# Kernel optimization log

Measured on AMD Instinct MI355X. Metric: run time of the kernel, lower is better.

## Reference

```python
import jax, jax.numpy as jnp
import numpy as np

Y_SCALE = 0.01  # fixed weight quantization scale (q_scale of the int8 weights)


def setup_inputs() -> dict:
    key = jax.random.key(0)
    kx, kw, kb = jax.random.split(key, 3)
    B, S, IN, OUT = 4, 2048, 4096, 4096
    x = jax.random.normal(kx, (B, S, IN), dtype=jnp.float32)
    # int8 quantized weights, stored transposed as (in_features, out_features)
    weight_q = jax.random.randint(kw, (IN, OUT), -128, 128, dtype=jnp.int32)
    bias = jax.random.normal(kb, (OUT,), dtype=jnp.float32)
    return {"x": x, "weight_q": weight_q, "bias": bias}


def reference(x, weight_q, bias):
    # Per-batch-sample dynamic activation scale: max(|x_i|)/128 over each [S, IN] slice
    x_scale = jnp.max(jnp.abs(x), axis=(1, 2), keepdims=True) / 128.0  # [B,1,1]
    # int8 quantize: round + clip
    xq = jnp.clip(jnp.round(x / x_scale), -128, 127).astype(jnp.int8)  # [B,S,IN]
    wq = weight_q.astype(jnp.int8)                                      # [IN,OUT]
    c = jax.lax.dot_general(
        xq, wq,
        dimension_numbers=(((2,), (0,)), ((), ())),
        preferred_element_type=jnp.int32,
    )  # [B,S,OUT]
    # dequantize and bias-add
    y = c.astype(jnp.float32) * (x_scale * Y_SCALE)
    return y + bias
```

## Files before the change

kernel.cpp:

```cpp
#include <hip/hip_runtime.h>
#include <stdint.h>

#define K_DIM 4096
#define N_DIM 4096
#define M_DIM 8192
#define S_ROWS 2048
#define NKT 64

typedef int v4i __attribute__((ext_vector_type(4)));

__device__ __forceinline__ void gload16(const void* g, void* l) {
    __builtin_amdgcn_global_load_lds(
        (const __attribute__((address_space(1))) unsigned int*)g,
        (__attribute__((address_space(3))) unsigned int*)l, 16, 0, 0);
}

__device__ __forceinline__ void barrier() {
    asm volatile("" ::: "memory");
    __builtin_amdgcn_s_barrier();
    asm volatile("" ::: "memory");
}

__global__ void prep1_kernel(const float* __restrict__ x, unsigned* __restrict__ amax,
                             const int* __restrict__ wq, char* __restrict__ wt) {
    __shared__ unsigned lds[64 * 17];
    if (blockIdx.x < 4096) {
        int b = blockIdx.x >> 10;
        int bx = blockIdx.x & 1023;
        const float4* xb = (const float4*)(x + (size_t)b * S_ROWS * K_DIM);
        int tid = bx * 256 + threadIdx.x;
        const int stride = 1024 * 256;
        float m = 0.f;
#pragma unroll
        for (int i = 0; i < 8; ++i) {
            float4 v = xb[tid + i * stride];
            m = fmaxf(m, fmaxf(fmaxf(fabsf(v.x), fabsf(v.y)),
                               fmaxf(fabsf(v.z), fabsf(v.w))));
        }
#pragma unroll
        for (int off = 32; off; off >>= 1)
            m = fmaxf(m, __shfl_xor(m, off));
        float* red = (float*)lds;
        if ((threadIdx.x & 63) == 0) red[threadIdx.x >> 6] = m;
        __syncthreads();
        if (threadIdx.x == 0) {
            m = fmaxf(fmaxf(red[0], red[1]), fmaxf(red[2], red[3]));
            atomicMax(&amax[b], __float_as_uint(m));
        }
    } else {
        int wb = blockIdx.x - 4096;
        int n0 = (wb & 63) * 64;
        int k0 = (wb >> 6) * 64;
        int t = threadIdx.x;
        int c = t & 63;
        int g = t >> 6;
#pragma unroll
        for (int rep = 0; rep < 4; ++rep) {
            int kb = g * 16 + rep * 4;
            int v0 = wq[(size_t)(k0 + kb + 0) * N_DIM + n0 + c];
            int v1 = wq[(size_t)(k0 + kb + 1) * N_DIM + n0 + c];
            int v2 = wq[(size_t)(k0 + kb + 2) * N_DIM + n0 + c];
            int v3 = wq[(size_t)(k0 + kb + 3) * N_DIM + n0 + c];
            lds[c * 17 + (kb >> 2)] =
                (v0 & 255) | ((v1 & 255) << 8) | ((v2 & 255) << 16) | ((v3 & 255) << 24);
        }
        __syncthreads();
        int row = t >> 2;
        int ch = t & 3;
        uint4 o;
        o.x = lds[row * 17 + ch * 4 + 0];
        o.y = lds[row * 17 + ch * 4 + 1];
        o.z = lds[row * 17 + ch * 4 + 2];
        o.w = lds[row * 17 + ch * 4 + 3];
        *(uint4*)(wt + (size_t)(n0 + row) * K_DIM + k0 + ch * 16) = o;
    }
}

__global__ void quant_kernel(const float* __restrict__ x,
                             const unsigned* __restrict__ amax,
                             char* __restrict__ xq) {
    size_t gid = (size_t)blockIdx.x * 256 + threadIdx.x;
    size_t base = gid * 16;
    int b = (int)(base >> 23);
    float inv = 128.0f / __uint_as_float(amax[b]);
    const float4* xs = (const float4*)(x + base);
    unsigned parts[4];
#pragma unroll
    for (int i = 0; i < 4; ++i) {
        float4 v = xs[i];
        int q0 = max(-128, min(127, (int)rintf(v.x * inv)));
        int q1 = max(-128, min(127, (int)rintf(v.y * inv)));
        int q2 = max(-128, min(127, (int)rintf(v.z * inv)));
        int q3 = max(-128, min(127, (int)rintf(v.w * inv)));
        parts[i] = (q0 & 255) | ((q1 & 255) << 8) | ((q2 & 255) << 16) | ((q3 & 255) << 24);
    }
    *(uint4*)(xq + base) = make_uint4(parts[0], parts[1], parts[2], parts[3]);
}

__global__ __launch_bounds__(512, 4) void gemm8_kernel(
    const char* __restrict__ A, const char* __restrict__ Bt,
    const float* __restrict__ bias, const unsigned* __restrict__ amax,
    float* __restrict__ out) {
    __shared__ char sm[73728];
    const int t = threadIdx.x;
    const int l = t & 63;
    const int w = t >> 6;
    const int wm = w >> 1;
    const int wn = w & 1;
    const int rb = l & 15;
    const int sg = l >> 4;

    int bid = blockIdx.x;
    int xcd = bid & 7;
    int idx = bid >> 3;
    int mt = (xcd << 2) | (idx >> 5);
    int nt = idx & 31;
    const size_t m0 = (size_t)mt * 256;
    const size_t n0 = (size_t)nt * 128;

    const int lineA = wm * 32 + (rb >> 1);
    const int lineB = wn * 32 + (rb >> 1);
    const int svBase = ((rb & 1) << 2) | sg;
    const int offA = lineA * 128 + ((svBase ^ (lineA & 7)) << 4);
    const int offB = 16384 + lineB * 128 + ((svBase ^ (lineB & 7)) << 4);

    v4i acc[4][4];
#pragma unroll
    for (int i = 0; i < 4; ++i)
#pragma unroll
        for (int j = 0; j < 4; ++j) acc[i][j] = (v4i){0, 0, 0, 0};

#define ST_FULL(tt, bsel)                                                    \
    if ((tt) < NKT) {                                                        \
        char* lb = sm + (bsel) * 24576;                                      \
        const char* ga = A + m0 * K_DIM + (size_t)(tt) * 64;                 \
        const char* gb = Bt + n0 * K_DIM + (size_t)(tt) * 64;                \
        _Pragma("unroll")                                                    \
        for (int j = 0; j < 2; ++j) {                                        \
            int p = j * 512 + t;                                             \
            int line = p >> 3, sl = p & 7;                                   \
            int sv = sl ^ (line & 7);                                        \
            int r = line * 2 + (sv >> 2), ks = sv & 3;                       \
            gload16(ga + (size_t)r * K_DIM + ks * 16, lb + p * 16);          \
        }                                                                    \
        {                                                                    \
            int p = t;                                                       \
            int line = p >> 3, sl = p & 7;                                   \
            int sv = sl ^ (line & 7);                                        \
            int r = line * 2 + (sv >> 2), ks = sv & 3;                       \
            gload16(gb + (size_t)r * K_DIM + ks * 16, lb + 16384 + p * 16);  \
        }                                                                    \
    }

    ST_FULL(0, 0);
    ST_FULL(1, 1);

    v4i aF[4], bF[4];
    int cur = 0;

    for (int i = 0; i < NKT; ++i) {
        if (i == NKT - 1) { asm volatile("s_waitcnt vmcnt(0)" ::: "memory"); }
        else             { asm volatile("s_waitcnt vmcnt(3)" ::: "memory"); }
        barrier();

        int s2 = cur + 2; if (s2 >= 3) s2 -= 3;
        ST_FULL(i + 2, s2);

        const char* pb = sm + cur * 24576;
        const char* pA = pb + offA;
        const char* pB = pb + offB;
#pragma unroll
        for (int ni = 0; ni < 4; ++ni) bF[ni] = *(const v4i*)(pB + ni * 1024);
#pragma unroll
        for (int mi = 0; mi < 4; ++mi) aF[mi] = *(const v4i*)(pA + mi * 1024);

        __builtin_amdgcn_s_setprio(1);
#pragma unroll
        for (int mi = 0; mi < 4; ++mi)
#pragma unroll
            for (int ni = 0; ni < 4; ++ni)
                acc[mi][ni] = __builtin_amdgcn_mfma_i32_16x16x64_i8(
                    aF[mi], bF[ni], acc[mi][ni], 0, 0, 0);
        __builtin_amdgcn_s_setprio(0);

        cur = (cur == 2) ? 0 : cur + 1;
    }

    float scale = __uint_as_float(amax[m0 >> 11]) * (1.0f / 128.0f) * 0.01f;
    float bv[4];
#pragma unroll
    for (int ni = 0; ni < 4; ++ni) bv[ni] = bias[n0 + wn * 64 + ni * 16 + rb];
#pragma unroll
    for (int mi = 0; mi < 4; ++mi) {
#pragma unroll
        for (int rg = 0; rg < 4; ++rg) {
            size_t row = m0 + wm * 64 + mi * 16 + sg * 4 + rg;
            float* orow = out + row * N_DIM + n0 + wn * 64 + rb;
#pragma unroll
            for (int ni = 0; ni < 4; ++ni)
                orow[ni * 16] = (float)acc[mi][ni][rg] * scale + bv[ni];
        }
    }
#undef ST_FULL
}

extern "C" void kernel_launch(void* const* d_in, const int* in_sizes, int n_in,
                              void* d_out, int out_size, void* d_ws, size_t ws_size,
                              hipStream_t stream) {
    const float* x = (const float*)d_in[0];
    const int* wq = (const int*)d_in[1];
    const float* bias = (const float*)d_in[2];
    float* out = (float*)d_out;

    unsigned* amax = (unsigned*)d_ws;
    char* xq = (char*)d_ws + 256;
    char* wt = (char*)d_ws + 256 + (size_t)M_DIM * K_DIM;

    hipMemsetAsync(d_ws, 0, 16, stream);

    prep1_kernel<<<dim3(8192), 256, 0, stream>>>(x, amax, wq, wt);
    quant_kernel<<<8192, 256, 0, stream>>>(x, amax, xq);
    gemm8_kernel<<<dim3(1024), 512, 0, stream>>>(xq, wt, bias, amax, out);
}
```

Before: 241.5 us.

## Pre-tile operands into MFMA fragment layout and load directly from global

The quantize and weight-transpose kernels now write A and B in a tiled layout where each 16-row by 64-k block is stored as contiguous 16-byte fragments, one per lane. The GEMM drops shared memory and barriers and loads MFMA fragments straight from global memory into registers with double-buffered register prefetch. Tiles shrink to 128x128 with 256 threads, and the grid doubles. This removes the LDS staging and synchronisation cost but loses cross-wave data sharing through LDS, so more operand traffic goes through L2/global.

Result: slower. 261.7 us (+8.4%).

```diff
diff --git a/kernel.cpp b/kernel.cpp
--- a/kernel.cpp
+++ b/kernel.cpp
@@ -5,21 +5,10 @@
 #define N_DIM 4096
 #define M_DIM 8192
 #define S_ROWS 2048
-#define NKT 64
+#define NKT 32
 
 typedef int v4i __attribute__((ext_vector_type(4)));
 
-__device__ __forceinline__ void gload16(const void* g, void* l) {
-    __builtin_amdgcn_global_load_lds(
-        (const __attribute__((address_space(1))) unsigned int*)g,
-        (__attribute__((address_space(3))) unsigned int*)l, 16, 0, 0);
-}
-
-__device__ __forceinline__ void barrier() {
-    asm volatile("" ::: "memory");
-    __builtin_amdgcn_s_barrier();
-    asm volatile("" ::: "memory");
-}
 
 __global__ void prep1_kernel(const float* __restrict__ x, unsigned* __restrict__ amax,
                              const int* __restrict__ wq, char* __restrict__ wt) {
@@ -50,17 +39,17 @@
     } else {
         int wb = blockIdx.x - 4096;
         int n0 = (wb & 63) * 64;
-        int k0 = (wb >> 6) * 64;
+        int k0b = (wb >> 6) * 64;
         int t = threadIdx.x;
         int c = t & 63;
         int g = t >> 6;
 #pragma unroll
         for (int rep = 0; rep < 4; ++rep) {
             int kb = g * 16 + rep * 4;
-            int v0 = wq[(size_t)(k0 + kb + 0) * N_DIM + n0 + c];
-            int v1 = wq[(size_t)(k0 + kb + 1) * N_DIM + n0 + c];
-            int v2 = wq[(size_t)(k0 + kb + 2) * N_DIM + n0 + c];
-            int v3 = wq[(size_t)(k0 + kb + 3) * N_DIM + n0 + c];
+            int v0 = wq[(size_t)(k0b + kb + 0) * N_DIM + n0 + c];
+            int v1 = wq[(size_t)(k0b + kb + 1) * N_DIM + n0 + c];
+            int v2 = wq[(size_t)(k0b + kb + 2) * N_DIM + n0 + c];
+            int v3 = wq[(size_t)(k0b + kb + 3) * N_DIM + n0 + c];
             lds[c * 17 + (kb >> 2)] =
                 (v0 & 255) | ((v1 & 255) << 8) | ((v2 & 255) << 16) | ((v3 & 255) << 24);
         }
@@ -72,7 +61,11 @@
         o.y = lds[row * 17 + ch * 4 + 1];
         o.z = lds[row * 17 + ch * 4 + 2];
         o.w = lds[row * 17 + ch * 4 + 3];
-        *(uint4*)(wt + (size_t)(n0 + row) * K_DIM + k0 + ch * 16) = o;
+        int n = n0 + row;
+        int k0 = k0b + ch * 16;
+        size_t dst = ((size_t)(n >> 4) * 64 + (k0 >> 6)) * 1024 +
+                     (size_t)((n & 15) + ((k0 >> 4) & 3) * 16) * 16;
+        *(uint4*)(wt + dst) = o;
     }
 }
 
@@ -94,14 +87,17 @@
         int q3 = max(-128, min(127, (int)rintf(v.w * inv)));
         parts[i] = (q0 & 255) | ((q1 & 255) << 8) | ((q2 & 255) << 16) | ((q3 & 255) << 24);
     }
-    *(uint4*)(xq + base) = make_uint4(parts[0], parts[1], parts[2], parts[3]);
-}
-
-__global__ __launch_bounds__(512, 4) void gemm8_kernel(
+    int m = (int)(base >> 12);
+    int k0 = (int)(base & 4095);
+    size_t dst = ((size_t)(m >> 4) * 64 + (k0 >> 6)) * 1024 +
+                 (size_t)((m & 15) + ((k0 >> 4) & 3) * 16) * 16;
+    *(uint4*)(xq + dst) = make_uint4(parts[0], parts[1], parts[2], parts[3]);
+}
+
+__global__ __launch_bounds__(256, 2) void gemmf_kernel(
     const char* __restrict__ A, const char* __restrict__ Bt,
     const float* __restrict__ bias, const unsigned* __restrict__ amax,
     float* __restrict__ out) {
-    __shared__ char sm[73728];
     const int t = threadIdx.x;
     const int l = t & 63;
     const int w = t >> 6;
@@ -113,16 +109,13 @@
     int bid = blockIdx.x;
     int xcd = bid & 7;
     int idx = bid >> 3;
-    int mt = (xcd << 2) | (idx >> 5);
-    int nt = idx & 31;
-    const size_t m0 = (size_t)mt * 256;
+    int nt = (xcd << 2) | (idx & 3);
+    int mt = idx >> 2;
+    const size_t m0 = (size_t)mt * 128;
     const size_t n0 = (size_t)nt * 128;
 
-    const int lineA = wm * 32 + (rb >> 1);
-    const int lineB = wn * 32 + (rb >> 1);
-    const int svBase = ((rb & 1) << 2) | sg;
-    const int offA = lineA * 128 + ((svBase ^ (lineA & 7)) << 4);
-    const int offB = 16384 + lineB * 128 + ((svBase ^ (lineB & 7)) << 4);
+    const char* aB = A + (((m0 >> 4) + wm * 4) * 64) * 1024 + l * 16;
+    const char* bB = Bt + (((n0 >> 4) + wn * 4) * 64) * 1024 + l * 16;
 
     v4i acc[4][4];
 #pragma unroll
@@ -130,60 +123,46 @@
 #pragma unroll
         for (int j = 0; j < 4; ++j) acc[i][j] = (v4i){0, 0, 0, 0};
 
-#define ST_FULL(tt, bsel)                                                    \
-    if ((tt) < NKT) {                                                        \
-        char* lb = sm + (bsel) * 24576;                                      \
-        const char* ga = A + m0 * K_DIM + (size_t)(tt) * 64;                 \
-        const char* gb = Bt + n0 * K_DIM + (size_t)(tt) * 64;                \
+    v4i aX[4][2], bX[4][2], aY[4][2], bY[4][2];
+
+#define LDF(bufA, bufB, tt)                                                  \
+    {                                                                        \
+        int kf = (tt) * 2;                                                   \
         _Pragma("unroll")                                                    \
-        for (int j = 0; j < 2; ++j) {                                        \
-            int p = j * 512 + t;                                             \
-            int line = p >> 3, sl = p & 7;                                   \
-            int sv = sl ^ (line & 7);                                        \
-            int r = line * 2 + (sv >> 2), ks = sv & 3;                       \
-            gload16(ga + (size_t)r * K_DIM + ks * 16, lb + p * 16);          \
+        for (int mi = 0; mi < 4; ++mi) {                                     \
+            bufA[mi][0] = *(const v4i*)(aB + mi * 65536 + (size_t)kf * 1024);\
+            bufA[mi][1] = *(const v4i*)(aB + mi * 65536 + (size_t)(kf + 1) * 1024); \
         }                                                                    \
-        {                                                                    \
-            int p = t;                                                       \
-            int line = p >> 3, sl = p & 7;                                   \
-            int sv = sl ^ (line & 7);                                        \
-            int r = line * 2 + (sv >> 2), ks = sv & 3;                       \
-            gload16(gb + (size_t)r * K_DIM + ks * 16, lb + 16384 + p * 16);  \
+        _Pragma("unroll")                                                    \
+        for (int ni = 0; ni < 4; ++ni) {                                     \
+            bufB[ni][0] = *(const v4i*)(bB + ni * 65536 + (size_t)kf * 1024);\
+            bufB[ni][1] = *(const v4i*)(bB + ni * 65536 + (size_t)(kf + 1) * 1024); \
         }                                                                    \
     }
 
-    ST_FULL(0, 0);
-    ST_FULL(1, 1);
-
-    v4i aF[4], bF[4];
-    int cur = 0;
-
-    for (int i = 0; i < NKT; ++i) {
-        if (i == NKT - 1) { asm volatile("s_waitcnt vmcnt(0)" ::: "memory"); }
-        else             { asm volatile("s_waitcnt vmcnt(3)" ::: "memory"); }
-        barrier();
-
-        int s2 = cur + 2; if (s2 >= 3) s2 -= 3;
-        ST_FULL(i + 2, s2);
-
-        const char* pb = sm + cur * 24576;
-        const char* pA = pb + offA;
-        const char* pB = pb + offB;
-#pragma unroll
-        for (int ni = 0; ni < 4; ++ni) bF[ni] = *(const v4i*)(pB + ni * 1024);
-#pragma unroll
-        for (int mi = 0; mi < 4; ++mi) aF[mi] = *(const v4i*)(pA + mi * 1024);
-
+#define MFMA_T(bufA, bufB)                                                   \
+    _Pragma("unroll")                                                        \
+    for (int mi = 0; mi < 4; ++mi)                                           \
+        _Pragma("unroll")                                                    \
+        for (int ni = 0; ni < 4; ++ni)                                       \
+            _Pragma("unroll")                                                \
+            for (int ks = 0; ks < 2; ++ks)                                   \
+                acc[mi][ni] = __builtin_amdgcn_mfma_i32_16x16x64_i8(         \
+                    bufA[mi][ks], bufB[ni][ks], acc[mi][ni], 0, 0, 0);
+
+    LDF(aX, bX, 0);
+    for (int kt = 0; kt < NKT; kt += 2) {
+        LDF(aY, bY, kt + 1);
         __builtin_amdgcn_s_setprio(1);
-#pragma unroll
-        for (int mi = 0; mi < 4; ++mi)
-#pragma unroll
-            for (int ni = 0; ni < 4; ++ni)
-                acc[mi][ni] = __builtin_amdgcn_mfma_i32_16x16x64_i8(
-                    aF[mi], bF[ni], acc[mi][ni], 0, 0, 0);
+        MFMA_T(aX, bX);
         __builtin_amdgcn_s_setprio(0);
-
-        cur = (cur == 2) ? 0 : cur + 1;
+        {
+            int nxt = (kt + 2 < NKT) ? (kt + 2) : (NKT - 1);
+            LDF(aX, bX, nxt);
+        }
+        __builtin_amdgcn_s_setprio(1);
+        MFMA_T(aY, bY);
+        __builtin_amdgcn_s_setprio(0);
     }
 
     float scale = __uint_as_float(amax[m0 >> 11]) * (1.0f / 128.0f) * 0.01f;
@@ -201,7 +180,8 @@
                 orow[ni * 16] = (float)acc[mi][ni][rg] * scale + bv[ni];
         }
     }
-#undef ST_FULL
+#undef LDF
+#undef MFMA_T
 }
 
 extern "C" void kernel_launch(void* const* d_in, const int* in_sizes, int n_in,
@@ -220,5 +200,5 @@
 
     prep1_kernel<<<dim3(8192), 256, 0, stream>>>(x, amax, wq, wt);
     quant_kernel<<<8192, 256, 0, stream>>>(x, amax, xq);
-    gemm8_kernel<<<dim3(1024), 512, 0, stream>>>(xq, wt, bias, amax, out);
-}
+    gemmf_kernel<<<dim3(2048), 256, 0, stream>>>(xq, wt, bias, amax, out);
+}
```
